# Performance work log

Measured on AMD Instinct MI355X. Metric: run time of the kernel, lower is better.

The kernel has to match this reference:

```python
import math
import jax, jax.numpy as jnp
import numpy as np

N_BITS = 8
QN = -(2 ** (N_BITS - 1)) + 1   # -127
QP = 2 ** (N_BITS - 1) - 1      # 127
MSB = 1 << (N_BITS - 1)         # 128
SHAPE = (4096, 8192)
FLIP_NUM = 3356  # ceil(numel * 1e-4)


def setup_inputs() -> dict:
    key = jax.random.key(0)
    k1, k2, k3 = jax.random.split(key, 3)
    weight = jax.random.normal(k1, SHAPE, dtype=jnp.float32) * 0.05
    # alpha ~ LSQ init scale magnitude: 2*mean|w|/sqrt(Qp) ~= 0.007; keep positive
    alpha = jax.random.uniform(k2, (1,), dtype=jnp.float32, minval=0.005, maxval=0.02)
    flip_idx = jax.random.randint(k3, (FLIP_NUM,), 0, SHAPE[0] * SHAPE[1], dtype=jnp.int64)
    return {"weight": weight, "alpha": alpha, "flip_idx": flip_idx}


def _grad_scale(x, g):
    # forward: x ; backward: grad * g
    xg = x * g
    return xg + jax.lax.stop_gradient(x - xg)


def _round_pass(x):
    # forward: round(x) ; backward: identity (STE)
    return x + jax.lax.stop_gradient(jnp.round(x) - x)


def reference(weight, alpha, flip_idx):
    numel = weight.size
    g = 1.0 / math.sqrt(numel * QP)
    alpha_c = jnp.maximum(alpha, 1e-4)           # alpha.data.clamp_(min=1e-4)
    a = _grad_scale(alpha_c, g)                  # [1], broadcasts
    q = jnp.clip(weight / a, QN, QP)             # clamp to [Qn, Qp]
    # bit-flip injection: XOR MSB of the truncated-int value at sampled indices,
    # done in-place on .data in torch (no autograd record) -> stop_gradient here
    qf = q.reshape(-1)
    v = qf[flip_idx]
    flipped = jnp.bitwise_xor(v.astype(jnp.int32), MSB).astype(qf.dtype)
    qf = qf.at[flip_idx].set(jax.lax.stop_gradient(flipped))
    q = qf.reshape(weight.shape)
    w_q = _round_pass(q) * a
    return w_q
```

## Files before the change

kernel.cpp:

```cpp
#include <hip/hip_runtime.h>

#define QN_F (-127.0f)
#define QP_F (127.0f)
#define MSB 128

typedef float f32x4 __attribute__((ext_vector_type(4)));

__global__ void quant_fused_kernel(const float* __restrict__ w,
                                   const float* __restrict__ alpha,
                                   const int* __restrict__ flip_idx,
                                   float* __restrict__ out,
                                   int n4, int nf) {
    const float a = fmaxf(alpha[0], 1e-4f);

    const int per_block = (n4 + gridDim.x - 1) / gridDim.x;
    const int lo4 = blockIdx.x * per_block;
    const int hi4 = min(lo4 + per_block, n4);

    const f32x4* __restrict__ w4 = (const f32x4*)w;
    f32x4* __restrict__ out4 = (f32x4*)out;

    #pragma unroll 4
    for (int i = lo4 + (int)threadIdx.x; i < hi4; i += (int)blockDim.x) {
        f32x4 v = w4[i];
        f32x4 r;
        r.x = rintf(fminf(fmaxf(v.x / a, QN_F), QP_F)) * a;
        r.y = rintf(fminf(fmaxf(v.y / a, QN_F), QP_F)) * a;
        r.z = rintf(fminf(fmaxf(v.z / a, QN_F), QP_F)) * a;
        r.w = rintf(fminf(fmaxf(v.w / a, QN_F), QP_F)) * a;
        __builtin_nontemporal_store(r, &out4[i]);
    }

    __syncthreads();

    const int loF = lo4 * 4;
    const int hiF = hi4 * 4;
    for (int t = (int)threadIdx.x; t < nf; t += (int)blockDim.x) {
        int i = flip_idx[t];
        if (i >= loF && i < hiF) {
            float q = fminf(fmaxf(w[i] / a, QN_F), QP_F);
            int qi = (int)q;
            qi ^= MSB;
            out[i] = (float)qi * a;
        }
    }
}

extern "C" void kernel_launch(void* const* d_in, const int* in_sizes, int n_in,
                              void* d_out, int out_size, void* d_ws, size_t ws_size,
                              hipStream_t stream) {
    const float* w = (const float*)d_in[0];
    const float* alpha = (const float*)d_in[1];
    const int* flip_idx = (const int*)d_in[2];
    float* out = (float*)d_out;

    const int n = in_sizes[0];
    const int nf = in_sizes[2];
    const int n4 = n / 4;

    const int block = 256;
    const int grid = 2048;
    quant_fused_kernel<<<grid, block, 0, stream>>>(w, alpha, flip_idx, out, n4, nf);
}
```

Measured before the change: 47.95 us.

## Switch to grid-stride interleaved partitioning with power-of-two flip ownership

Replaces the contiguous per-block chunking with a grid-stride loop, so at every step all blocks access adjacent memory, and peels the remainder into a guarded tail. Ownership of each flip index is now computed with a mask on the global stride, which assumes the stride (grid times block) is a power of two. The intent is a more uniform DRAM access pattern and a simpler unrolled main loop. The flip pass still makes every block scan all flip indices, and each write must land on an element that the same block already stored.

New measurement: 50.00 us. +4.3%, slower.

```diff
diff --git a/kernel.cpp b/kernel.cpp
--- a/kernel.cpp
+++ b/kernel.cpp
@@ -6,22 +6,24 @@
 
 typedef float f32x4 __attribute__((ext_vector_type(4)));
 
-__global__ void quant_fused_kernel(const float* __restrict__ w,
-                                   const float* __restrict__ alpha,
-                                   const int* __restrict__ flip_idx,
-                                   float* __restrict__ out,
-                                   int n4, int nf) {
+__global__ void __launch_bounds__(256)
+quant_fused_kernel(const float* __restrict__ w,
+                   const float* __restrict__ alpha,
+                   const int* __restrict__ flip_idx,
+                   float* __restrict__ out,
+                   int n4, int nf) {
     const float a = fmaxf(alpha[0], 1e-4f);
-
-    const int per_block = (n4 + gridDim.x - 1) / gridDim.x;
-    const int lo4 = blockIdx.x * per_block;
-    const int hi4 = min(lo4 + per_block, n4);
+    const int stride = gridDim.x * blockDim.x;
+    const int idx = blockIdx.x * blockDim.x + threadIdx.x;
 
     const f32x4* __restrict__ w4 = (const f32x4*)w;
     f32x4* __restrict__ out4 = (f32x4*)out;
 
+    const int nfull = n4 / stride;
+    int k = 0;
     #pragma unroll 4
-    for (int i = lo4 + (int)threadIdx.x; i < hi4; i += (int)blockDim.x) {
+    for (; k < nfull; ++k) {
+        const int i = idx + k * stride;
         f32x4 v = w4[i];
         f32x4 r;
         r.x = rintf(fminf(fmaxf(v.x / a, QN_F), QP_F)) * a;
@@ -30,18 +32,30 @@
         r.w = rintf(fminf(fmaxf(v.w / a, QN_F), QP_F)) * a;
         __builtin_nontemporal_store(r, &out4[i]);
     }
+    {
+        const int i = idx + k * stride;
+        if (i < n4) {
+            f32x4 v = w4[i];
+            f32x4 r;
+            r.x = rintf(fminf(fmaxf(v.x / a, QN_F), QP_F)) * a;
+            r.y = rintf(fminf(fmaxf(v.y / a, QN_F), QP_F)) * a;
+            r.z = rintf(fminf(fmaxf(v.z / a, QN_F), QP_F)) * a;
+            r.w = rintf(fminf(fmaxf(v.w / a, QN_F), QP_F)) * a;
+            __builtin_nontemporal_store(r, &out4[i]);
+        }
+    }
 
     __syncthreads();
 
-    const int loF = lo4 * 4;
-    const int hiF = hi4 * 4;
+    const unsigned smask = (unsigned)stride - 1u;
     for (int t = (int)threadIdx.x; t < nf; t += (int)blockDim.x) {
-        int i = flip_idx[t];
-        if (i >= loF && i < hiF) {
-            float q = fminf(fmaxf(w[i] / a, QN_F), QP_F);
+        const int e = flip_idx[t];
+        const unsigned owner = (((unsigned)e >> 2) & smask) / blockDim.x;
+        if (owner == blockIdx.x) {
+            float q = fminf(fmaxf(w[e] / a, QN_F), QP_F);
             int qi = (int)q;
             qi ^= MSB;
-            out[i] = (float)qi * a;
+            out[e] = (float)qi * a;
         }
     }
 }
```
